# Optimization experiments

Hardware: AMD Instinct MI355X
Metric: run time of the kernel (lower is better)

The kernel has to match this reference:

```python
import jax, jax.numpy as jnp
import numpy as np

B, S, D = 2, 2048, 1024
H = 16
HD = D // H

def setup_inputs() -> dict:
    key = jax.random.key(0)
    k1, k2, k3 = jax.random.split(key, 3)
    # xavier-uniform-ish scale for weights
    x = jax.random.normal(k1, (B, S, D), dtype=jnp.float32)
    lim_qkv = np.sqrt(6.0 / (D + 3 * D)).astype(np.float32)
    lim_o = np.sqrt(6.0 / (D + D)).astype(np.float32)
    qkv_w = jax.random.uniform(k2, (3 * D, D), minval=-lim_qkv, maxval=lim_qkv, dtype=jnp.float32)
    o_w = jax.random.uniform(k3, (D, D), minval=-lim_o, maxval=lim_o, dtype=jnp.float32)
    qkv_b = jnp.zeros((3 * D,), dtype=jnp.float32)
    o_b = jnp.zeros((D,), dtype=jnp.float32)
    return {"x": x, "qkv_w": qkv_w, "qkv_b": qkv_b, "o_w": o_w, "o_b": o_b}

def reference(x, qkv_w, qkv_b, o_w, o_b):
    b, s, _ = x.shape
    # qkv projection: Linear(input_dim, 3*embed_dim)
    qkv = jnp.einsum('bsd,ed->bse', x, qkv_w) + qkv_b          # [B,S,3D]
    qkv = qkv.reshape(b, s, H, 3 * HD).transpose(0, 2, 1, 3)    # [B,H,S,3*HD]
    q, k, v = jnp.split(qkv, 3, axis=-1)                        # each [B,H,S,HD]
    scale = 1.0 / np.sqrt(HD).astype(np.float32)
    scores = jnp.einsum('bhqd,bhkd->bhqk', q, k) * scale        # [B,H,S,S]
    attn = jax.nn.softmax(scores, axis=-1)
    vals = jnp.einsum('bhqk,bhkd->bhqd', attn, v)               # [B,H,S,HD]
    vals = vals.transpose(0, 2, 1, 3).reshape(b, s, H * HD)     # [B,S,D]
    o = jnp.einsum('bse,de->bsd', vals, o_w) + o_b              # [B,S,D]
    return o
```

## Files before the change

### kernel.cpp

```cpp
#include <hip/hip_runtime.h>
#include <math.h>
#include <stdint.h>

typedef _Float16 half_t;
typedef _Float16 f16x8 __attribute__((ext_vector_type(8)));
typedef _Float16 f16x4 __attribute__((ext_vector_type(4)));
typedef _Float16 f16x2 __attribute__((ext_vector_type(2)));
typedef float    f32x4 __attribute__((ext_vector_type(4)));
typedef float    f32x16 __attribute__((ext_vector_type(16)));
typedef unsigned int u32x2 __attribute__((ext_vector_type(2)));

__device__ __forceinline__ void gload16(const void* g, void* l) {
    __builtin_amdgcn_global_load_lds(
        (const __attribute__((address_space(1))) void*)(uintptr_t)g,
        (__attribute__((address_space(3))) void*)(uint32_t)(uintptr_t)l,
        16, 0, 0);
}

__device__ __forceinline__ float fast_exp2(float x) {
#if __has_builtin(__builtin_amdgcn_exp2f)
    return __builtin_amdgcn_exp2f(x);
#else
    return exp2f(x);
#endif
}
__device__ __forceinline__ unsigned cvt2h_u32(float a, float b) {
#if __has_builtin(__builtin_amdgcn_cvt_pkrtz)
    union { __fp16 __attribute__((ext_vector_type(2))) s; unsigned d; } u;
    u.s = __builtin_amdgcn_cvt_pkrtz(a, b);
    return u.d;
#else
    union { f16x2 s; unsigned d; } u;
    u.s = (f16x2){ (half_t)a, (half_t)b };
    return u.d;
#endif
}

#define QSCALE 0.18033688011112042f

__global__ __launch_bounds__(256)
void cvt3_kernel(const float* __restrict__ a, half_t* __restrict__ da, int na,
                 const float* __restrict__ b, half_t* __restrict__ db, int nb,
                 const float* __restrict__ c, half_t* __restrict__ dc)
{
    int i = blockIdx.x * 256 + threadIdx.x;
    const float* s; half_t* d; int off;
    if (i < na)           { s = a; d = da; off = i; }
    else if (i < na + nb) { s = b; d = db; off = i - na; }
    else                  { s = c; d = dc; off = i - na - nb; }
    float4 v = reinterpret_cast<const float4*>(s)[off];
    f16x4 h = { (half_t)v.x, (half_t)v.y, (half_t)v.z, (half_t)v.w };
    reinterpret_cast<f16x4*>(d)[off] = h;
}

template<int BM, int BN, int MODE, int MINWG, int DBUF>
__global__ __launch_bounds__(256, MINWG)
void gemm_kernel(const half_t* __restrict__ A,
                 const half_t* __restrict__ Bw,
                 const float* __restrict__ bias,
                 void* __restrict__ outp,
                 half_t* __restrict__ kout,
                 half_t* __restrict__ vtout,
                 int N, int K, int nbx)
{
    constexpr int CA = BM / 32, CB = BN / 32;
    constexpr int MW = BM / 2,  NW = BN / 2;
    constexpr int IF = MW / 16, JF = NW / 16;
    constexpr int AE = BM * 64, BE = BN * 64;
    constexpr int NB = DBUF ? 2 : 1;

    __shared__ half_t As[NB * AE];
    __shared__ half_t Bs[NB * BE];

    const int tid  = threadIdx.x;
    const int lane = tid & 63;
    const int w    = tid >> 6;
    const int wm   = w >> 1, wn = w & 1;
    const int lr   = lane & 15, lg = lane >> 4;
    const int swk  = lr & 7;

    const int nwg = gridDim.x;
    const int cpx = nwg >> 3;
    const int swz = (blockIdx.x & 7) * cpx + (blockIdx.x >> 3);
    const int m0  = (swz % nbx) * BM;
    const int n0  = (swz / nbx) * BN;

    const int srow = lane >> 3;
    const int scol = ((lane & 7) ^ srow) * 8;

    f32x4 acc[JF][IF] = {};

    if constexpr (!DBUF) {
        for (int k0 = 0; k0 < K; k0 += 64) {
            #pragma unroll
            for (int c = 0; c < CA; ++c) {
                const int chunk = w * CA + c;
                const int row   = chunk * 8 + srow;
                gload16(&A[(size_t)(m0 + row) * K + k0 + scol], &As[chunk * 512]);
            }
            #pragma unroll
            for (int c = 0; c < CB; ++c) {
                const int chunk = w * CB + c;
                const int row   = chunk * 8 + srow;
                gload16(&Bw[(size_t)(n0 + row) * K + k0 + scol], &Bs[chunk * 512]);
            }
            __syncthreads();

            #pragma unroll
            for (int kk = 0; kk < 2; ++kk) {
                f16x8 af[IF], bf[JF];
                #pragma unroll
                for (int i = 0; i < IF; ++i)
                    af[i] = *reinterpret_cast<const f16x8*>(
                        &As[(wm*MW + i*16 + lr) * 64 + (((kk*4 + lg) ^ swk) << 3)]);
                #pragma unroll
                for (int j = 0; j < JF; ++j)
                    bf[j] = *reinterpret_cast<const f16x8*>(
                        &Bs[(wn*NW + j*16 + lr) * 64 + (((kk*4 + lg) ^ swk) << 3)]);
                #pragma unroll
                for (int j = 0; j < JF; ++j)
                    #pragma unroll
                    for (int i = 0; i < IF; ++i)
                        acc[j][i] = __builtin_amdgcn_mfma_f32_16x16x32_f16(bf[j], af[i], acc[j][i], 0, 0, 0);
            }
            __syncthreads();
        }
    } else {
        const int NT = K >> 6;
        #pragma unroll
        for (int c = 0; c < CA; ++c) {
            const int chunk = w * CA + c;
            const int row   = chunk * 8 + srow;
            gload16(&A[(size_t)(m0 + row) * K + scol], &As[chunk * 512]);
        }
        #pragma unroll
        for (int c = 0; c < CB; ++c) {
            const int chunk = w * CB + c;
            const int row   = chunk * 8 + srow;
            gload16(&Bw[(size_t)(n0 + row) * K + scol], &Bs[chunk * 512]);
        }
        __syncthreads();

        int cur = 0;
        for (int kt = 0; kt < NT; ++kt) {
            if (kt + 1 < NT) {
                const int k1 = (kt + 1) << 6;
                #pragma unroll
                for (int c = 0; c < CA; ++c) {
                    const int chunk = w * CA + c;
                    const int row   = chunk * 8 + srow;
                    gload16(&A[(size_t)(m0 + row) * K + k1 + scol], &As[(cur ^ 1) * AE + chunk * 512]);
                }
                #pragma unroll
                for (int c = 0; c < CB; ++c) {
                    const int chunk = w * CB + c;
                    const int row   = chunk * 8 + srow;
                    gload16(&Bw[(size_t)(n0 + row) * K + k1 + scol], &Bs[(cur ^ 1) * BE + chunk * 512]);
                }
            }
            #pragma unroll
            for (int kk = 0; kk < 2; ++kk) {
                f16x8 af[IF], bf[JF];
                #pragma unroll
                for (int i = 0; i < IF; ++i)
                    af[i] = *reinterpret_cast<const f16x8*>(
                        &As[cur * AE + (wm*MW + i*16 + lr) * 64 + (((kk*4 + lg) ^ swk) << 3)]);
                #pragma unroll
                for (int j = 0; j < JF; ++j)
                    bf[j] = *reinterpret_cast<const f16x8*>(
                        &Bs[cur * BE + (wn*NW + j*16 + lr) * 64 + (((kk*4 + lg) ^ swk) << 3)]);
                #pragma unroll
                for (int j = 0; j < JF; ++j)
                    #pragma unroll
                    for (int i = 0; i < IF; ++i)
                        acc[j][i] = __builtin_amdgcn_mfma_f32_16x16x32_f16(bf[j], af[i], acc[j][i], 0, 0, 0);
            }
            if (kt + 1 < NT) __syncthreads();
            cur ^= 1;
        }
    }

    #pragma unroll
    for (int j = 0; j < JF; ++j) {
        const int nb = n0 + wn*NW + j*16 + lg*4;
        const float4 bv = *reinterpret_cast<const float4*>(&bias[nb]);
        #pragma unroll
        for (int i = 0; i < IF; ++i) {
            const int gm = m0 + wm*MW + i*16 + lr;
            f32x4 v = acc[j][i];
            v[0] += bv.x; v[1] += bv.y; v[2] += bv.z; v[3] += bv.w;
            if (MODE == 1) {
                float4 st = { v[0], v[1], v[2], v[3] };
                *reinterpret_cast<float4*>(&((float*)outp)[(size_t)gm * N + nb]) = st;
            } else {
                const int b = gm >> 11, s = gm & 2047;
                const int h = nb / 192, cc = nb % 192;
                const int t = cc >> 6, d = cc & 63;
                const size_t bh = (size_t)(b * 16 + h);
                if (t == 0) {
                    f16x4 hv = { (half_t)(v[0]*QSCALE), (half_t)(v[1]*QSCALE),
                                 (half_t)(v[2]*QSCALE), (half_t)(v[3]*QSCALE) };
                    *reinterpret_cast<f16x4*>(&((half_t*)outp)[(bh*2048 + s)*64 + d]) = hv;
                } else if (t == 1) {
                    f16x4 hv = { (half_t)v[0], (half_t)v[1], (half_t)v[2], (half_t)v[3] };
                    *reinterpret_cast<f16x4*>(&kout[(bh*2048 + s)*64 + d]) = hv;
                } else {
                    #pragma unroll
                    for (int r = 0; r < 4; ++r)
                        vtout[(bh*64 + d + r)*2048 + s] = (half_t)v[r];
                }
            }
        }
    }
}

__global__ __launch_bounds__(512, 2)
void attn_kernel(const half_t* __restrict__ qb,
                 const half_t* __restrict__ kb,
                 const half_t* __restrict__ vtb,
                 half_t* __restrict__ vals)
{
    __shared__ __attribute__((aligned(16))) char buf[49152];
    half_t* KtH = (half_t*)buf;
    half_t* VtH = (half_t*)(buf + 24576);

    const int tid  = threadIdx.x;
    const int lane = tid & 63;
    const int w    = tid >> 6;
    const int wq   = w & 3;
    const int kh   = w >> 2;
    const int q32  = lane & 31;
    const int hi   = lane >> 5;
    const int i    = blockIdx.x;
    const int bh   = (i & 7) * 4 + ((i >> 3) & 3);
    const int qblk = i >> 5;
    const int b    = bh >> 4, h = bh & 15;
    const size_t base = (size_t)bh * 2048 * 64;
    const int q0 = qblk * 128;
    const int swk = lane & 7;

    f16x8 qf[4];
    {
        const int qr = q0 + wq*32 + q32;
        #pragma unroll
        for (int kd = 0; kd < 4; ++kd)
            qf[kd] = *reinterpret_cast<const f16x8*>(&qb[base + (size_t)qr*64 + kd*16 + hi*8]);
    }

    const int srow = tid >> 3;
    const int ssl  = (tid & 7) ^ (srow & 7);
    const half_t* kg = kb  + base + (size_t)srow * 64   + ssl * 8;
    const half_t* vg = vtb + base + (size_t)srow * 2048 + ssl * 8;
    const int ldst = w * 512;

    f32x16 acco[2] = {};
    float l_run = 0.0f;

    #pragma unroll
    for (int tt = 0; tt < 3; ++tt) {
        gload16(kg + (size_t)tt * 4096, &KtH[tt * 4096 + ldst]);
        gload16(vg + tt * 64,           &VtH[tt * 4096 + ldst]);
    }

    int bi = 0;
    for (int t = 0; t < 32; ++t) {
        const int rem = 31 - t;
        if (rem >= 2)      asm volatile("s_waitcnt vmcnt(4)" ::: "memory");
        else if (rem == 1) asm volatile("s_waitcnt vmcnt(2)" ::: "memory");
        else               asm volatile("s_waitcnt vmcnt(0)" ::: "memory");
        __builtin_amdgcn_s_barrier();
        __builtin_amdgcn_sched_barrier(0);

        const half_t* Kc = &KtH[bi * 4096];
        const half_t* Vc = &VtH[bi * 4096];

        f32x16 accs = {};
        __builtin_amdgcn_s_setprio(1);
        #pragma unroll
        for (int kd = 0; kd < 4; ++kd) {
            const f16x8 kf = *reinterpret_cast<const f16x8*>(
                &Kc[(kh*32 + q32) * 64 + (((kd*2 + hi) ^ swk) << 3)]);
            accs = __builtin_amdgcn_mfma_f32_32x32x16_f16(kf, qf[kd], accs, 0, 0, 0);
        }
        __builtin_amdgcn_s_setprio(0);

        unsigned P2[8];
        float psum = 0.0f;
        #pragma unroll
        for (int p = 0; p < 8; ++p) {
            const float pa = fast_exp2(accs[2*p]);
            const float pb = fast_exp2(accs[2*p+1]);
            psum += pa + pb;
            P2[p] = cvt2h_u32(pa, pb);
        }
        l_run += psum;

        __builtin_amdgcn_s_setprio(1);
        #pragma unroll
        for (int kb2 = 0; kb2 < 2; ++kb2) {
            const u32x2 s0 = __builtin_amdgcn_permlane32_swap(P2[4*kb2+0], P2[4*kb2+2], false, false);
            const u32x2 s1 = __builtin_amdgcn_permlane32_swap(P2[4*kb2+1], P2[4*kb2+3], false, false);
            union { unsigned u[4]; f16x8 v; } pf;
            pf.u[0] = s0[0]; pf.u[1] = s1[0]; pf.u[2] = s0[1]; pf.u[3] = s1[1];
            #pragma unroll
            for (int d2 = 0; d2 < 2; ++d2) {
                const f16x8 vf = *reinterpret_cast<const f16x8*>(
                    &Vc[(d2*32 + q32) * 64 + (((kh*4 + kb2*2 + hi) ^ swk) << 3)]);
                acco[d2] = __builtin_amdgcn_mfma_f32_32x32x16_f16(vf, pf.v, acco[d2], 0, 0, 0);
            }
        }
        __builtin_amdgcn_s_setprio(0);

        __builtin_amdgcn_s_barrier();
        if (t < 29) {
            gload16(kg + (size_t)(t + 3) * 4096, &KtH[bi * 4096 + ldst]);
            gload16(vg + (t + 3) * 64,           &VtH[bi * 4096 + ldst]);
        }
        bi = (bi == 2) ? 0 : bi + 1;
    }

    l_run += __shfl_xor(l_run, 32);

    float* mrg = (float*)buf;
    __syncthreads();
    if (kh == 1) {
        float* dst = &mrg[(wq*64 + lane) * 33];
        #pragma unroll
        for (int d2 = 0; d2 < 2; ++d2)
            #pragma unroll
            for (int r = 0; r < 16; ++r) dst[d2*16 + r] = acco[d2][r];
        dst[32] = l_run;
    }
    __syncthreads();
    if (kh == 0) {
        const float* src = &mrg[(wq*64 + lane) * 33];
        const float inv_l = 1.0f / (l_run + src[32]);
        const int row = b*2048 + q0 + wq*32 + q32;
        #pragma unroll
        for (int d2 = 0; d2 < 2; ++d2) {
            #pragma unroll
            for (int rq = 0; rq < 4; ++rq) {
                const int dbase = d2*32 + rq*8 + hi*4;
                f16x4 hv;
                #pragma unroll
                for (int j = 0; j < 4; ++j) {
                    const int r = rq*4 + j;
                    hv[j] = (half_t)((acco[d2][r] + src[d2*16 + r]) * inv_l);
                }
                *reinterpret_cast<f16x4*>(&vals[(size_t)row*1024 + h*64 + dbase]) = hv;
            }
        }
    }
}

extern "C" void kernel_launch(void* const* d_in, const int* in_sizes, int n_in,
                              void* d_out, int out_size, void* d_ws, size_t ws_size,
                              hipStream_t stream)
{
    const float* x     = (const float*)d_in[0];
    const float* qkv_w = (const float*)d_in[1];
    const float* qkv_b = (const float*)d_in[2];
    const float* o_w   = (const float*)d_in[3];
    const float* o_b   = (const float*)d_in[4];
    float* out = (float*)d_out;

    const size_t M1 = (size_t)1024 * 1024;
    half_t* x16   = (half_t*)d_ws;
    half_t* w16   = x16   + 4 * M1;
    half_t* ow16  = w16   + 3 * M1;
    half_t* qbuf  = ow16  + 1 * M1;
    half_t* kbuf  = qbuf  + 4 * M1;
    half_t* vtbuf = kbuf  + 4 * M1;
    half_t* vals  = vtbuf + 4 * M1;

    cvt3_kernel<<<8192, 256, 0, stream>>>(x, x16, 1048576, qkv_w, w16, 786432, o_w, ow16);
    gemm_kernel<128, 128, 0, 3, 0><<<768, 256, 0, stream>>>(
        x16, w16, qkv_b, qbuf, kbuf, vtbuf, 3072, 1024, 32);
    attn_kernel<<<512, 512, 0, stream>>>(qbuf, kbuf, vtbuf, vals);
    gemm_kernel<128, 64, 1, 2, 1><<<512, 256, 0, stream>>>(
        vals, ow16, o_b, out, nullptr, nullptr, 1024, 1024, 32);
}
```

Baseline: 101.8 us.

## Use four-stage K/V ring in attention to drop trailing barrier, grid-stride conversion

The attention kernel's shared K/V staging grows from a 3-slot to a 4-slot ring. The prefetch for tile t+3 is now issued right after the top-of-loop barrier into a slot not being read, which removes the second barrier per iteration. The softmax row sum now comes from packed fp16 dot2 instructions on the already-converted probabilities. The fp32-to-fp16 conversion kernel becomes a grid-stride loop with a quarter of the blocks. The larger LDS footprint (64KB per 512-thread block) may reduce how many blocks fit per CU, and summing the rounded fp16 values slightly changes the normalisation.

```diff
diff --git a/kernel.cpp b/kernel.cpp
--- a/kernel.cpp
+++ b/kernel.cpp
@@ -6,6 +6,7 @@
 typedef _Float16 f16x8 __attribute__((ext_vector_type(8)));
 typedef _Float16 f16x4 __attribute__((ext_vector_type(4)));
 typedef _Float16 f16x2 __attribute__((ext_vector_type(2)));
+typedef __fp16   fp16x2 __attribute__((ext_vector_type(2)));
 typedef float    f32x4 __attribute__((ext_vector_type(4)));
 typedef float    f32x16 __attribute__((ext_vector_type(16)));
 typedef unsigned int u32x2 __attribute__((ext_vector_type(2)));
@@ -26,7 +27,7 @@
 }
 __device__ __forceinline__ unsigned cvt2h_u32(float a, float b) {
 #if __has_builtin(__builtin_amdgcn_cvt_pkrtz)
-    union { __fp16 __attribute__((ext_vector_type(2))) s; unsigned d; } u;
+    union { fp16x2 s; unsigned d; } u;
     u.s = __builtin_amdgcn_cvt_pkrtz(a, b);
     return u.d;
 #else
@@ -35,22 +36,34 @@
     return u.d;
 #endif
 }
+__device__ __forceinline__ float dot2_acc(unsigned p2, float acc) {
+#if __has_builtin(__builtin_amdgcn_fdot2)
+    union { unsigned u; fp16x2 h; } c; c.u = p2;
+    const fp16x2 ones = { (__fp16)1.0f, (__fp16)1.0f };
+    return __builtin_amdgcn_fdot2(c.h, ones, acc, false);
+#else
+    union { unsigned u; f16x2 h; } c; c.u = p2;
+    return acc + (float)c.h[0] + (float)c.h[1];
+#endif
+}
 
 #define QSCALE 0.18033688011112042f
 
 __global__ __launch_bounds__(256)
 void cvt3_kernel(const float* __restrict__ a, half_t* __restrict__ da, int na,
                  const float* __restrict__ b, half_t* __restrict__ db, int nb,
-                 const float* __restrict__ c, half_t* __restrict__ dc)
+                 const float* __restrict__ c, half_t* __restrict__ dc, int nc)
 {
-    int i = blockIdx.x * 256 + threadIdx.x;
-    const float* s; half_t* d; int off;
-    if (i < na)           { s = a; d = da; off = i; }
-    else if (i < na + nb) { s = b; d = db; off = i - na; }
-    else                  { s = c; d = dc; off = i - na - nb; }
-    float4 v = reinterpret_cast<const float4*>(s)[off];
-    f16x4 h = { (half_t)v.x, (half_t)v.y, (half_t)v.z, (half_t)v.w };
-    reinterpret_cast<f16x4*>(d)[off] = h;
+    const int total = na + nb + nc;
+    for (int i = blockIdx.x * 256 + threadIdx.x; i < total; i += gridDim.x * 256) {
+        const float* s; half_t* d; int off;
+        if (i < na)           { s = a; d = da; off = i; }
+        else if (i < na + nb) { s = b; d = db; off = i - na; }
+        else                  { s = c; d = dc; off = i - na - nb; }
+        float4 v = reinterpret_cast<const float4*>(s)[off];
+        f16x4 h = { (half_t)v.x, (half_t)v.y, (half_t)v.z, (half_t)v.w };
+        reinterpret_cast<f16x4*>(d)[off] = h;
+    }
 }
 
 template<int BM, int BN, int MODE, int MINWG, int DBUF>
@@ -220,9 +233,9 @@
                  const half_t* __restrict__ vtb,
                  half_t* __restrict__ vals)
 {
-    __shared__ __attribute__((aligned(16))) char buf[49152];
+    __shared__ __attribute__((aligned(16))) char buf[65536];
     half_t* KtH = (half_t*)buf;
-    half_t* VtH = (half_t*)(buf + 24576);
+    half_t* VtH = (half_t*)(buf + 32768);
 
     const int tid  = threadIdx.x;
     const int lane = tid & 63;
@@ -262,8 +275,8 @@
         gload16(vg + tt * 64,           &VtH[tt * 4096 + ldst]);
     }
 
-    int bi = 0;
     for (int t = 0; t < 32; ++t) {
+        const int bi = t & 3;
         const int rem = 31 - t;
         if (rem >= 2)      asm volatile("s_waitcnt vmcnt(4)" ::: "memory");
         else if (rem == 1) asm volatile("s_waitcnt vmcnt(2)" ::: "memory");
@@ -271,6 +284,12 @@
         __builtin_amdgcn_s_barrier();
         __builtin_amdgcn_sched_barrier(0);
 
+        if (t <= 28) {
+            const int sb = (t + 3) & 3;
+            gload16(kg + (size_t)(t + 3) * 4096, &KtH[sb * 4096 + ldst]);
+            gload16(vg + (t + 3) * 64,           &VtH[sb * 4096 + ldst]);
+        }
+
         const half_t* Kc = &KtH[bi * 4096];
         const half_t* Vc = &VtH[bi * 4096];
 
@@ -290,8 +309,8 @@
         for (int p = 0; p < 8; ++p) {
             const float pa = fast_exp2(accs[2*p]);
             const float pb = fast_exp2(accs[2*p+1]);
-            psum += pa + pb;
             P2[p] = cvt2h_u32(pa, pb);
+            psum = dot2_acc(P2[p], psum);
         }
         l_run += psum;
 
@@ -310,13 +329,6 @@
             }
         }
         __builtin_amdgcn_s_setprio(0);
-
-        __builtin_amdgcn_s_barrier();
-        if (t < 29) {
-            gload16(kg + (size_t)(t + 3) * 4096, &KtH[bi * 4096 + ldst]);
-            gload16(vg + (t + 3) * 64,           &VtH[bi * 4096 + ldst]);
-        }
-        bi = (bi == 2) ? 0 : bi + 1;
     }
 
     l_run += __shfl_xor(l_run, 32);
@@ -373,7 +385,7 @@
     half_t* vtbuf = kbuf  + 4 * M1;
     half_t* vals  = vtbuf + 4 * M1;
 
-    cvt3_kernel<<<8192, 256, 0, stream>>>(x, x16, 1048576, qkv_w, w16, 786432, o_w, ow16);
+    cvt3_kernel<<<2048, 256, 0, stream>>>(x, x16, 1048576, qkv_w, w16, 786432, o_w, ow16, 262144);
     gemm_kernel<128, 128, 0, 3, 0><<<768, 256, 0, stream>>>(
         x16, w16, qkv_b, qbuf, kbuf, vtbuf, 3072, 1024, 32);
     attn_kernel<<<512, 512, 0, stream>>>(qbuf, kbuf, vtbuf, vals);
```

New measurement: 101.8 us. Within noise of the previous version (-0.0%).

## Add 256x256 pipelined QKV GEMM with staggered async loads and grid-stride conversion

Applied to the files above, without the earlier changes.

Replaces the 128x128 single-buffered QKV projection GEMM with a dedicated 256x256-tile, 512-thread kernel. It double-buffers LDS and interleaves global-to-LDS loads of the next tiles between MFMA phases, using explicit vmcnt waits, raw barriers and setprio. The aim is to hide load latency and raise operand reuse. The fp32-to-fp16 conversion kernel becomes grid-stride with fewer blocks. The trade-off is a grid of only 192 blocks (under one wave on 256 CUs) and large LDS use per block.

```diff
diff --git a/kernel.cpp b/kernel.cpp
--- a/kernel.cpp
+++ b/kernel.cpp
@@ -6,6 +6,7 @@
 typedef _Float16 f16x8 __attribute__((ext_vector_type(8)));
 typedef _Float16 f16x4 __attribute__((ext_vector_type(4)));
 typedef _Float16 f16x2 __attribute__((ext_vector_type(2)));
+typedef __fp16   fp16x2 __attribute__((ext_vector_type(2)));
 typedef float    f32x4 __attribute__((ext_vector_type(4)));
 typedef float    f32x16 __attribute__((ext_vector_type(16)));
 typedef unsigned int u32x2 __attribute__((ext_vector_type(2)));
@@ -26,7 +27,7 @@
 }
 __device__ __forceinline__ unsigned cvt2h_u32(float a, float b) {
 #if __has_builtin(__builtin_amdgcn_cvt_pkrtz)
-    union { __fp16 __attribute__((ext_vector_type(2))) s; unsigned d; } u;
+    union { fp16x2 s; unsigned d; } u;
     u.s = __builtin_amdgcn_cvt_pkrtz(a, b);
     return u.d;
 #else
@@ -41,36 +42,158 @@
 __global__ __launch_bounds__(256)
 void cvt3_kernel(const float* __restrict__ a, half_t* __restrict__ da, int na,
                  const float* __restrict__ b, half_t* __restrict__ db, int nb,
-                 const float* __restrict__ c, half_t* __restrict__ dc)
+                 const float* __restrict__ c, half_t* __restrict__ dc, int nc)
 {
-    int i = blockIdx.x * 256 + threadIdx.x;
-    const float* s; half_t* d; int off;
-    if (i < na)           { s = a; d = da; off = i; }
-    else if (i < na + nb) { s = b; d = db; off = i - na; }
-    else                  { s = c; d = dc; off = i - na - nb; }
-    float4 v = reinterpret_cast<const float4*>(s)[off];
-    f16x4 h = { (half_t)v.x, (half_t)v.y, (half_t)v.z, (half_t)v.w };
-    reinterpret_cast<f16x4*>(d)[off] = h;
-}
-
-template<int BM, int BN, int MODE, int MINWG, int DBUF>
+    const int total = na + nb + nc;
+    for (int i = blockIdx.x * 256 + threadIdx.x; i < total; i += gridDim.x * 256) {
+        const float* s; half_t* d; int off;
+        if (i < na)           { s = a; d = da; off = i; }
+        else if (i < na + nb) { s = b; d = db; off = i - na; }
+        else                  { s = c; d = dc; off = i - na - nb; }
+        float4 v = reinterpret_cast<const float4*>(s)[off];
+        f16x4 h = { (half_t)v.x, (half_t)v.y, (half_t)v.z, (half_t)v.w };
+        reinterpret_cast<f16x4*>(d)[off] = h;
+    }
+}
+
+__global__ __launch_bounds__(512, 2)
+void gemm256_kernel(const half_t* __restrict__ A,
+                    const half_t* __restrict__ Bw,
+                    const float* __restrict__ bias,
+                    half_t* __restrict__ qout,
+                    half_t* __restrict__ kout,
+                    half_t* __restrict__ vtout)
+{
+    constexpr int K = 1024;
+    __shared__ half_t As[2 * 16384];
+    __shared__ half_t Bs[2 * 16384];
+
+    const int tid  = threadIdx.x;
+    const int lane = tid & 63;
+    const int w    = tid >> 6;
+    const int wm   = w >> 2, wn = w & 3;
+    const int lr   = lane & 15, lg = lane >> 4;
+    const int swk  = lr & 7;
+
+    const int swz = ((int)blockIdx.x & 7) * 24 + ((int)blockIdx.x >> 3);
+    const int m0  = (swz & 15) * 256;
+    const int n0  = (swz >> 4) * 256;
+
+    const int srow = lane >> 3;
+    const int scol = ((lane & 7) ^ srow) * 8;
+
+    f32x4 acc[4][8] = {};
+
+    #define STAGE_A(kt, h)  do { \
+        const int db_ = (kt) & 1; \
+        _Pragma("unroll") \
+        for (int r_ = 0; r_ < 2; ++r_) { \
+            const int row_ = (h)*128 + w*16 + r_*8 + srow; \
+            gload16(&A[(size_t)(m0 + row_) * K + (kt)*64 + scol], \
+                    &As[db_*16384 + (h)*8192 + (w*2 + r_)*512]); \
+        } } while (0)
+    #define STAGE_B(kt, h)  do { \
+        const int db_ = (kt) & 1; \
+        _Pragma("unroll") \
+        for (int r_ = 0; r_ < 2; ++r_) { \
+            const int row_ = (h)*128 + w*16 + r_*8 + srow; \
+            gload16(&Bw[(size_t)(n0 + row_) * K + (kt)*64 + scol], \
+                    &Bs[db_*16384 + (h)*8192 + (w*2 + r_)*512]); \
+        } } while (0)
+
+    STAGE_A(0, 0); STAGE_A(0, 1); STAGE_B(0, 0); STAGE_B(0, 1); STAGE_A(1, 0);
+
+    for (int T = 0; T < 16; ++T) {
+        const int db = T & 1;
+        const half_t* Ab = &As[db * 16384];
+        const half_t* Bb = &Bs[db * 16384];
+
+        if (T < 15) asm volatile("s_waitcnt vmcnt(2)" ::: "memory");
+        else        asm volatile("s_waitcnt vmcnt(0)" ::: "memory");
+        if (T + 1 < 16) STAGE_A(T + 1, 1);
+        __builtin_amdgcn_s_barrier();
+        __builtin_amdgcn_sched_barrier(0);
+
+        #pragma unroll
+        for (int p = 0; p < 4; ++p) {
+            const int ih = p & 1;
+            const int kk = p >> 1;
+            f16x8 af[4], bf[4];
+            #pragma unroll
+            for (int i4 = 0; i4 < 4; ++i4) {
+                const int row = wm*128 + (ih*4 + i4)*16 + lr;
+                af[i4] = *reinterpret_cast<const f16x8*>(
+                    &Ab[row*64 + (((kk*4 + lg) ^ swk) << 3)]);
+            }
+            #pragma unroll
+            for (int j = 0; j < 4; ++j) {
+                const int row = wn*64 + j*16 + lr;
+                bf[j] = *reinterpret_cast<const f16x8*>(
+                    &Bb[row*64 + (((kk*4 + lg) ^ swk) << 3)]);
+            }
+            if (p == 1 && T + 1 < 16) STAGE_B(T + 1, 0);
+            if (p == 2 && T + 1 < 16) STAGE_B(T + 1, 1);
+            if (p == 3 && T + 2 < 16) STAGE_A(T + 2, 0);
+
+            __builtin_amdgcn_s_setprio(1);
+            #pragma unroll
+            for (int j = 0; j < 4; ++j)
+                #pragma unroll
+                for (int i4 = 0; i4 < 4; ++i4)
+                    acc[j][ih*4 + i4] = __builtin_amdgcn_mfma_f32_16x16x32_f16(
+                        bf[j], af[i4], acc[j][ih*4 + i4], 0, 0, 0);
+            __builtin_amdgcn_s_setprio(0);
+
+            if (p >= 2) __builtin_amdgcn_s_barrier();
+        }
+    }
+    #undef STAGE_A
+    #undef STAGE_B
+
+    #pragma unroll
+    for (int j = 0; j < 4; ++j) {
+        const int nb = n0 + wn*64 + j*16 + lg*4;
+        const float4 bv = *reinterpret_cast<const float4*>(&bias[nb]);
+        #pragma unroll
+        for (int i = 0; i < 8; ++i) {
+            const int gm = m0 + wm*128 + i*16 + lr;
+            f32x4 v = acc[j][i];
+            v[0] += bv.x; v[1] += bv.y; v[2] += bv.z; v[3] += bv.w;
+            const int b = gm >> 11, s = gm & 2047;
+            const int h = nb / 192, cc = nb % 192;
+            const int t = cc >> 6, d = cc & 63;
+            const size_t bh = (size_t)(b * 16 + h);
+            if (t == 0) {
+                f16x4 hv = { (half_t)(v[0]*QSCALE), (half_t)(v[1]*QSCALE),
+                             (half_t)(v[2]*QSCALE), (half_t)(v[3]*QSCALE) };
+                *reinterpret_cast<f16x4*>(&qout[(bh*2048 + s)*64 + d]) = hv;
+            } else if (t == 1) {
+                f16x4 hv = { (half_t)v[0], (half_t)v[1], (half_t)v[2], (half_t)v[3] };
+                *reinterpret_cast<f16x4*>(&kout[(bh*2048 + s)*64 + d]) = hv;
+            } else {
+                #pragma unroll
+                for (int r = 0; r < 4; ++r)
+                    vtout[(bh*64 + d + r)*2048 + s] = (half_t)v[r];
+            }
+        }
+    }
+}
+
+template<int BM, int BN, int MINWG>
 __global__ __launch_bounds__(256, MINWG)
 void gemm_kernel(const half_t* __restrict__ A,
                  const half_t* __restrict__ Bw,
                  const float* __restrict__ bias,
-                 void* __restrict__ outp,
-                 half_t* __restrict__ kout,
-                 half_t* __restrict__ vtout,
+                 float* __restrict__ outp,
                  int N, int K, int nbx)
 {
     constexpr int CA = BM / 32, CB = BN / 32;
     constexpr int MW = BM / 2,  NW = BN / 2;
     constexpr int IF = MW / 16, JF = NW / 16;
     constexpr int AE = BM * 64, BE = BN * 64;
-    constexpr int NB = DBUF ? 2 : 1;
-
-    __shared__ half_t As[NB * AE];
-    __shared__ half_t Bs[NB * BE];
+
+    __shared__ half_t As[2 * AE];
+    __shared__ half_t Bs[2 * BE];
 
     const int tid  = threadIdx.x;
     const int lane = tid & 63;
@@ -89,95 +212,58 @@
     const int scol = ((lane & 7) ^ srow) * 8;
 
     f32x4 acc[JF][IF] = {};
-
-    if constexpr (!DBUF) {
-        for (int k0 = 0; k0 < K; k0 += 64) {
+    const int NT = K >> 6;
+
+    #pragma unroll
+    for (int c = 0; c < CA; ++c) {
+        const int chunk = w * CA + c;
+        const int row   = chunk * 8 + srow;
+        gload16(&A[(size_t)(m0 + row) * K + scol], &As[chunk * 512]);
+    }
+    #pragma unroll
+    for (int c = 0; c < CB; ++c) {
+        const int chunk = w * CB + c;
+        const int row   = chunk * 8 + srow;
+        gload16(&Bw[(size_t)(n0 + row) * K + scol], &Bs[chunk * 512]);
+    }
+    __syncthreads();
+
+    int cur = 0;
+    for (int kt = 0; kt < NT; ++kt) {
+        if (kt + 1 < NT) {
+            const int k1 = (kt + 1) << 6;
             #pragma unroll
             for (int c = 0; c < CA; ++c) {
                 const int chunk = w * CA + c;
                 const int row   = chunk * 8 + srow;
-                gload16(&A[(size_t)(m0 + row) * K + k0 + scol], &As[chunk * 512]);
+                gload16(&A[(size_t)(m0 + row) * K + k1 + scol], &As[(cur ^ 1) * AE + chunk * 512]);
             }
             #pragma unroll
             for (int c = 0; c < CB; ++c) {
                 const int chunk = w * CB + c;
                 const int row   = chunk * 8 + srow;
-                gload16(&Bw[(size_t)(n0 + row) * K + k0 + scol], &Bs[chunk * 512]);
-            }
-            __syncthreads();
-
-            #pragma unroll
-            for (int kk = 0; kk < 2; ++kk) {
-                f16x8 af[IF], bf[JF];
+                gload16(&Bw[(size_t)(n0 + row) * K + k1 + scol], &Bs[(cur ^ 1) * BE + chunk * 512]);
+            }
+        }
+        #pragma unroll
+        for (int kk = 0; kk < 2; ++kk) {
+            f16x8 af[IF], bf[JF];
+            #pragma unroll
+            for (int i = 0; i < IF; ++i)
+                af[i] = *reinterpret_cast<const f16x8*>(
+                    &As[cur * AE + (wm*MW + i*16 + lr) * 64 + (((kk*4 + lg) ^ swk) << 3)]);
+            #pragma unroll
+            for (int j = 0; j < JF; ++j)
+                bf[j] = *reinterpret_cast<const f16x8*>(
+                    &Bs[cur * BE + (wn*NW + j*16 + lr) * 64 + (((kk*4 + lg) ^ swk) << 3)]);
+            #pragma unroll
+            for (int j = 0; j < JF; ++j)
                 #pragma unroll
                 for (int i = 0; i < IF; ++i)
-                    af[i] = *reinterpret_cast<const f16x8*>(
-                        &As[(wm*MW + i*16 + lr) * 64 + (((kk*4 + lg) ^ swk) << 3)]);
-                #pragma unroll
-                for (int j = 0; j < JF; ++j)
-                    bf[j] = *reinterpret_cast<const f16x8*>(
-                        &Bs[(wn*NW + j*16 + lr) * 64 + (((kk*4 + lg) ^ swk) << 3)]);
-                #pragma unroll
-                for (int j = 0; j < JF; ++j)
-                    #pragma unroll
-                    for (int i = 0; i < IF; ++i)
-                        acc[j][i] = __builtin_amdgcn_mfma_f32_16x16x32_f16(bf[j], af[i], acc[j][i], 0, 0, 0);
-            }
-            __syncthreads();
-        }
-    } else {
-        const int NT = K >> 6;
-        #pragma unroll
-        for (int c = 0; c < CA; ++c) {
-            const int chunk = w * CA + c;
-            const int row   = chunk * 8 + srow;
-            gload16(&A[(size_t)(m0 + row) * K + scol], &As[chunk * 512]);
-        }
-        #pragma unroll
-        for (int c = 0; c < CB; ++c) {
-            const int chunk = w * CB + c;
-            const int row   = chunk * 8 + srow;
-            gload16(&Bw[(size_t)(n0 + row) * K + scol], &Bs[chunk * 512]);
-        }
-        __syncthreads();
-
-        int cur = 0;
-        for (int kt = 0; kt < NT; ++kt) {
-            if (kt + 1 < NT) {
-                const int k1 = (kt + 1) << 6;
-                #pragma unroll
-                for (int c = 0; c < CA; ++c) {
-                    const int chunk = w * CA + c;
-                    const int row   = chunk * 8 + srow;
-                    gload16(&A[(size_t)(m0 + row) * K + k1 + scol], &As[(cur ^ 1) * AE + chunk * 512]);
-                }
-                #pragma unroll
-                for (int c = 0; c < CB; ++c) {
-                    const int chunk = w * CB + c;
-                    const int row   = chunk * 8 + srow;
-                    gload16(&Bw[(size_t)(n0 + row) * K + k1 + scol], &Bs[(cur ^ 1) * BE + chunk * 512]);
-                }
-            }
-            #pragma unroll
-            for (int kk = 0; kk < 2; ++kk) {
-                f16x8 af[IF], bf[JF];
-                #pragma unroll
-                for (int i = 0; i < IF; ++i)
-                    af[i] = *reinterpret_cast<const f16x8*>(
-                        &As[cur * AE + (wm*MW + i*16 + lr) * 64 + (((kk*4 + lg) ^ swk) << 3)]);
-                #pragma unroll
-                for (int j = 0; j < JF; ++j)
-                    bf[j] = *reinterpret_cast<const f16x8*>(
-                        &Bs[cur * BE + (wn*NW + j*16 + lr) * 64 + (((kk*4 + lg) ^ swk) << 3)]);
-                #pragma unroll
-                for (int j = 0; j < JF; ++j)
-                    #pragma unroll
-                    for (int i = 0; i < IF; ++i)
-                        acc[j][i] = __builtin_amdgcn_mfma_f32_16x16x32_f16(bf[j], af[i], acc[j][i], 0, 0, 0);
-            }
-            if (kt + 1 < NT) __syncthreads();
-            cur ^= 1;
-        }
+                    acc[j][i] = __builtin_amdgcn_mfma_f32_16x16x32_f16(bf[j], af[i], acc[j][i], 0, 0, 0);
+        }
+        if (kt + 1 < NT) __syncthreads();
+        cur ^= 1;
     }
 
     #pragma unroll
@@ -189,27 +275,8 @@
             const int gm = m0 + wm*MW + i*16 + lr;
             f32x4 v = acc[j][i];
             v[0] += bv.x; v[1] += bv.y; v[2] += bv.z; v[3] += bv.w;
-            if (MODE == 1) {
-                float4 st = { v[0], v[1], v[2], v[3] };
-                *reinterpret_cast<float4*>(&((float*)outp)[(size_t)gm * N + nb]) = st;
-            } else {
-                const int b = gm >> 11, s = gm & 2047;
-                const int h = nb / 192, cc = nb % 192;
-                const int t = cc >> 6, d = cc & 63;
-                const size_t bh = (size_t)(b * 16 + h);
-                if (t == 0) {
-                    f16x4 hv = { (half_t)(v[0]*QSCALE), (half_t)(v[1]*QSCALE),
-                                 (half_t)(v[2]*QSCALE), (half_t)(v[3]*QSCALE) };
-                    *reinterpret_cast<f16x4*>(&((half_t*)outp)[(bh*2048 + s)*64 + d]) = hv;
-                } else if (t == 1) {
-                    f16x4 hv = { (half_t)v[0], (half_t)v[1], (half_t)v[2], (half_t)v[3] };
-                    *reinterpret_cast<f16x4*>(&kout[(bh*2048 + s)*64 + d]) = hv;
-                } else {
-                    #pragma unroll
-                    for (int r = 0; r < 4; ++r)
-                        vtout[(bh*64 + d + r)*2048 + s] = (half_t)v[r];
-                }
-            }
+            float4 st = { v[0], v[1], v[2], v[3] };
+            *reinterpret_cast<float4*>(&outp[(size_t)gm * N + nb]) = st;
         }
     }
 }
@@ -373,10 +440,9 @@
     half_t* vtbuf = kbuf  + 4 * M1;
     half_t* vals  = vtbuf + 4 * M1;
 
-    cvt3_kernel<<<8192, 256, 0, stream>>>(x, x16, 1048576, qkv_w, w16, 786432, o_w, ow16);
-    gemm_kernel<128, 128, 0, 3, 0><<<768, 256, 0, stream>>>(
-        x16, w16, qkv_b, qbuf, kbuf, vtbuf, 3072, 1024, 32);
+    cvt3_kernel<<<2048, 256, 0, stream>>>(x, x16, 1048576, qkv_w, w16, 786432, o_w, ow16, 262144);
+    gemm256_kernel<<<192, 512, 0, stream>>>(x16, w16, qkv_b, qbuf, kbuf, vtbuf);
     attn_kernel<<<512, 512, 0, stream>>>(qbuf, kbuf, vtbuf, vals);
-    gemm_kernel<128, 64, 1, 2, 1><<<512, 256, 0, stream>>>(
-        vals, ow16, o_b, out, nullptr, nullptr, 1024, 1024, 32);
-}
+    gemm_kernel<128, 64, 2><<<512, 256, 0, stream>>>(
+        vals, ow16, o_b, out, 1024, 1024, 32);
+}
```

Result: slower. 105.6 us (+3.7%).
